# Optimization experiments

Hardware: AMD Instinct MI355X
Metric: run time of the kernel (lower is better)

## Reference

```python
import jax, jax.numpy as jnp
import numpy as np

N = 262144      # number of points
K = 16          # KNN neighbors -> fixed degree CSR
E = N * K
CLASS_DIM = 40


def setup_inputs() -> dict:
    key = jax.random.key(0)
    ks = jax.random.split(key, 12)
    x = jax.random.normal(ks[0], (N, 3), dtype=jnp.float32)
    indptr = (jnp.arange(N + 1, dtype=jnp.int32) * K)
    indices = jax.random.randint(ks[1], (E,), 0, N, dtype=jnp.int32)

    def xavier(k, fan_out, fan_in):
        bound = np.sqrt(6.0 / (fan_in + fan_out)).astype(np.float32)
        return jax.random.uniform(k, (fan_out, fan_in), dtype=jnp.float32,
                                  minval=-bound, maxval=bound)

    return {
        "x": x, "indptr": indptr, "indices": indices,
        "w1": xavier(ks[2], 64, 3),
        "w2": xavier(ks[3], 64, 64),
        "w3": xavier(ks[4], 64, 64),
        "w4": xavier(ks[5], 128, 64),
        "w5": xavier(ks[6], 1024, 192),
        "wf1": xavier(ks[7], 512, 1024),
        "wf2": xavier(ks[8], 256, 512),
        "wf3": xavier(ks[9], CLASS_DIM, 256),
    }


def reference(x, indptr, indices, w1, w2, w3, w4, w5, wf1, wf2, wf3):
    # mlp1, mlp2 (bias-free Linear + ReLU)
    h = jax.nn.relu(x @ w1.T)          # [N, 64]
    h = jax.nn.relu(h @ w2.T)          # [N, 64]

    # GraphMaxPooling: CSR neighbor max (segment-max over gathered rows)
    n = h.shape[0]
    e = indices.shape[0]
    deg = indptr[1:] - indptr[:-1]                                   # [N]
    seg = jnp.repeat(jnp.arange(n, dtype=jnp.int32), deg,
                     total_repeat_length=e)                          # [E]
    x_gm = jax.ops.segment_max(h[indices], seg, num_segments=n,
                               indices_are_sorted=True)              # [N, 64]

    # mlp3, mlp4
    h3 = jax.nn.relu(h @ w3.T)         # [N, 64]
    h4 = jax.nn.relu(h3 @ w4.T)        # [N, 128]

    # concat neighbor-pooled features with point features, mlp5
    hc = jnp.concatenate([x_gm, h4], axis=1)   # [N, 192]
    h5 = jax.nn.relu(hc @ w5.T)                # [N, 1024]

    # global max pool over points -> [1, 1024]
    g = jnp.max(h5, axis=0, keepdims=True)

    # classifier head (dropout in eval mode = identity)
    f = jax.nn.relu(g @ wf1.T)
    f = jax.nn.relu(f @ wf2.T)
    return f @ wf3.T                            # [1, class_dim]
```

## Files before the change

### kernel.cpp

```cpp
#include <hip/hip_runtime.h>
#include <hip/hip_bf16.h>
#include <stdint.h>

typedef unsigned short u16;
typedef __bf16 bf16x8 __attribute__((ext_vector_type(8)));
typedef float  f32x4  __attribute__((ext_vector_type(4)));
typedef u16    u16x8  __attribute__((ext_vector_type(8)));

__device__ __forceinline__ float bf2f(u16 u) {
    return __uint_as_float(((unsigned)u) << 16);
}
__device__ __forceinline__ u16 f2bf(float f) {
    unsigned u = __float_as_uint(f);
    u += 0x7fffu + ((u >> 16) & 1u);
    return (u16)(u >> 16);
}
__device__ __forceinline__ u16x8 maxu16(u16x8 a, u16x8 b) {
    u16x8 r;
    #pragma unroll
    for (int e = 0; e < 8; ++e) r[e] = a[e] > b[e] ? a[e] : b[e];
    return r;
}

#define MFMA16(a, b, c) __builtin_amdgcn_mfma_f32_16x16x32_bf16(a, b, c, 0, 0, 0)

__device__ u16   h2g_buf[262144 * 64];
__device__ u16   gm_buf [262144 * 64];
__device__ u16   w3b[64 * 64];
__device__ u16   w4b[128 * 64];
__device__ u16   w5t[64 * 6 * 64 * 8];
__device__ float g_buf[1024];
__device__ float f1_buf[512];
__device__ float f2_buf[256];

__global__ void k0_zero() { g_buf[threadIdx.x] = 0.f; }

__global__ void kcvt(const float* __restrict__ w3f, const float* __restrict__ w4f,
                     const float* __restrict__ w5f)
{
    int i = blockIdx.x * 256 + threadIdx.x;
    if (i < 4096)        w3b[i]        = f2bf(w3f[i]);
    else if (i < 12288)  w4b[i - 4096] = f2bf(w4f[i - 4096]);
    else {
        int o    = i - 12288;
        int e    = o & 7;
        int lane = (o >> 3) & 63;
        int sg   = o >> 9;
        int s    = sg % 6, c16 = sg / 6;
        int q    = lane >> 4, l15 = lane & 15;
        w5t[o] = f2bf(w5f[(c16 * 16 + l15) * 192 + s * 32 + q * 8 + e]);
    }
}

__global__ __launch_bounds__(256) void k1_mlp(
    const float* __restrict__ xf, const float* __restrict__ w1f,
    const float* __restrict__ w2f)
{
    __shared__ __align__(16) u16 sw1[64 * 4];
    __shared__ __align__(16) u16 sx [64 * 4];
    __shared__ __align__(16) u16 sw2[64 * 72];
    __shared__ __align__(16) u16 shA[64 * 72];
    __shared__ __align__(16) u16 sh2[64 * 72];

    const int tid = threadIdx.x;
    const int p0  = blockIdx.x * 64;

    for (int i = tid; i < 64 * 64; i += 256)
        sw2[(i >> 6) * 72 + (i & 63)] = f2bf(w2f[i]);
    if (tid < 192) {
        sw1[(tid / 3) * 4 + tid % 3] = f2bf(w1f[tid]);
        sx [(tid / 3) * 4 + tid % 3] = f2bf(xf[p0 * 3 + tid]);
    }
    __syncthreads();

    {
        int m = tid & 63, ng = tid >> 6;
        float x0 = bf2f(sx[m * 4]), x1 = bf2f(sx[m * 4 + 1]), x2 = bf2f(sx[m * 4 + 2]);
        #pragma unroll
        for (int j = 0; j < 16; ++j) {
            int n = ng * 16 + j;
            float s = x0 * bf2f(sw1[n * 4]) + x1 * bf2f(sw1[n * 4 + 1]) + x2 * bf2f(sw1[n * 4 + 2]);
            shA[m * 72 + n] = f2bf(fmaxf(s, 0.f));
        }
    }
    __syncthreads();

    const int lane = tid & 63, w = tid >> 6, q = lane >> 4, l15 = lane & 15;
    const int mrow = 16 * w;

    f32x4 acc2[4];
    #pragma unroll
    for (int nt = 0; nt < 4; ++nt) acc2[nt] = (f32x4){0.f, 0.f, 0.f, 0.f};
    #pragma unroll
    for (int s = 0; s < 2; ++s) {
        bf16x8 a = *(const bf16x8*)&shA[(mrow + l15) * 72 + s * 32 + q * 8];
        #pragma unroll
        for (int nt = 0; nt < 4; ++nt) {
            bf16x8 b = *(const bf16x8*)&sw2[(nt * 16 + l15) * 72 + s * 32 + q * 8];
            acc2[nt] = MFMA16(a, b, acc2[nt]);
        }
    }
    #pragma unroll
    for (int nt = 0; nt < 4; ++nt)
        #pragma unroll
        for (int r = 0; r < 4; ++r) {
            int m = mrow + q * 4 + r;
            sh2[m * 72 + nt * 16 + l15] = f2bf(fmaxf(acc2[nt][r], 0.f));
        }
    __syncthreads();

    {
        int row = tid >> 2, c = (tid & 3) * 16;
        *(u16x8*)&h2g_buf[(size_t)p0 * 64 + tid * 16]     = *(const u16x8*)&sh2[row * 72 + c];
        *(u16x8*)&h2g_buf[(size_t)p0 * 64 + tid * 16 + 8] = *(const u16x8*)&sh2[row * 72 + c + 8];
    }
}

__global__ __launch_bounds__(256) void k2_pool(const int* __restrict__ idx)
{
    const size_t gt = (size_t)blockIdx.x * 256 + threadIdx.x;
    const size_t p  = gt >> 3;
    const int    c  = (threadIdx.x & 7) * 8;

    u16x8 v[16];
    #pragma unroll
    for (int k = 0; k < 16; ++k) {
        int j = idx[p * 16 + k];
        v[k] = *(const u16x8*)&h2g_buf[(size_t)j * 64 + c];
    }
    u16x8 m = v[0];
    #pragma unroll
    for (int k = 1; k < 16; ++k) m = maxu16(m, v[k]);
    *(u16x8*)&gm_buf[p * 64 + c] = m;
}

__global__ __launch_bounds__(512) void k3_fused(int* __restrict__ gout)
{
    __shared__ __align__(16) u16 lds[36864];
    u16* p0  = lds;
    u16* p1  = lds + 8192;
    u16* p2  = lds + 16384;
    u16* sw3 = lds + 24576;
    u16* sw4 = lds + 28672;

    const int tid  = threadIdx.x;
    const int lane = tid & 63, w = tid >> 6, q = lane >> 4, l15 = lane & 15;
    const size_t R0 = (size_t)blockIdx.x * 128;

    {
        int r = tid >> 3, js = tid & 7;
        *(u16x8*)&sw3[r * 64 + ((js ^ r) & 7) * 8] = *(const u16x8*)&w3b[r * 64 + js * 8];
        #pragma unroll
        for (int c = 0; c < 2; ++c) {
            int i = c * 512 + tid, r4 = i >> 3, j4 = i & 7;
            *(u16x8*)&sw4[r4 * 64 + ((j4 ^ r4) & 7) * 8] = *(const u16x8*)&w4b[r4 * 64 + j4 * 8];
        }
        #pragma unroll
        for (int c = 0; c < 2; ++c) {
            int i = c * 512 + tid, ra = i >> 3, ja = i & 7;
            *(u16x8*)&p0[ra * 64 + ((ja ^ ra) & 7) * 8] =
                *(const u16x8*)&gm_buf[(R0 + ra) * 64 + ja * 8];
            *(u16x8*)&p1[ra * 64 + ((ja ^ ra) & 7) * 8] =
                *(const u16x8*)&h2g_buf[(R0 + ra) * 64 + ja * 8];
        }
    }
    __syncthreads();

    {
        f32x4 a3[4];
        #pragma unroll
        for (int nt = 0; nt < 4; ++nt) a3[nt] = (f32x4){0.f, 0.f, 0.f, 0.f};
        #pragma unroll
        for (int ss = 0; ss < 2; ++ss) {
            int js = ss * 4 + q, r = w * 16 + l15;
            bf16x8 a = *(const bf16x8*)&p1[r * 64 + ((js ^ r) & 7) * 8];
            #pragma unroll
            for (int nt = 0; nt < 4; ++nt) {
                int rw = nt * 16 + l15;
                bf16x8 b = *(const bf16x8*)&sw3[rw * 64 + ((js ^ rw) & 7) * 8];
                a3[nt] = MFMA16(a, b, a3[nt]);
            }
        }
        #pragma unroll
        for (int nt = 0; nt < 4; ++nt)
            #pragma unroll
            for (int r = 0; r < 4; ++r) {
                int m = w * 16 + q * 4 + r;
                int n = nt * 16 + l15;
                p2[m * 64 + (((n >> 3) ^ m) & 7) * 8 + (n & 7)] =
                    f2bf(fmaxf(a3[nt][r], 0.f));
            }
    }

    {
        f32x4 a4[8];
        #pragma unroll
        for (int nt = 0; nt < 8; ++nt) a4[nt] = (f32x4){0.f, 0.f, 0.f, 0.f};
        #pragma unroll
        for (int ss = 0; ss < 2; ++ss) {
            int js = ss * 4 + q, r = w * 16 + l15;
            bf16x8 a = *(const bf16x8*)&p2[r * 64 + ((js ^ r) & 7) * 8];
            #pragma unroll
            for (int nt = 0; nt < 8; ++nt) {
                int rw = nt * 16 + l15;
                bf16x8 b = *(const bf16x8*)&sw4[rw * 64 + ((js ^ rw) & 7) * 8];
                a4[nt] = MFMA16(a, b, a4[nt]);
            }
        }
        #pragma unroll
        for (int nt = 0; nt < 8; ++nt)
            #pragma unroll
            for (int r = 0; r < 4; ++r) {
                int m  = w * 16 + q * 4 + r;
                int n4 = nt * 16 + l15;
                int j  = (n4 >> 3) & 7;
                u16* dp = (nt < 4) ? p1 : p2;
                dp[m * 64 + ((j ^ m) & 7) * 8 + (n4 & 7)] = f2bf(fmaxf(a4[nt][r], 0.f));
            }
    }
    __syncthreads();

    int zoff = 0;
    #pragma unroll 1
    for (int cg = 0; cg < 4; ++cg) {
        asm volatile("" : "+v"(zoff));
        f32x4 acc[8][2];
        #pragma unroll
        for (int mt = 0; mt < 8; ++mt)
            #pragma unroll
            for (int nt = 0; nt < 2; ++nt) acc[mt][nt] = (f32x4){0.f, 0.f, 0.f, 0.f};
        #pragma unroll
        for (int s = 0; s < 6; ++s) {
            const u16* pa = (s < 2) ? p0 : ((s < 4) ? p1 : p2);
            int j = (s & 1) * 4 + q;
            bf16x8 b[2];
            #pragma unroll
            for (int nt = 0; nt < 2; ++nt)
                b[nt] = *(const bf16x8*)&w5t[(size_t)(((cg * 16 + w * 2 + nt) * 6 + s)) * 512 + lane * 8];
            bf16x8 a[8];
            #pragma unroll
            for (int mt = 0; mt < 8; ++mt) {
                int r = mt * 16 + l15;
                a[mt] = *(const bf16x8*)&pa[r * 64 + ((j ^ r) & 7) * 8 + zoff];
            }
            #pragma unroll
            for (int mt = 0; mt < 8; ++mt)
                #pragma unroll
                for (int nt = 0; nt < 2; ++nt)
                    acc[mt][nt] = MFMA16(a[mt], b[nt], acc[mt][nt]);
        }

        #pragma unroll
        for (int nt = 0; nt < 2; ++nt) {
            float mx = 0.f;
            #pragma unroll
            for (int mt = 0; mt < 8; ++mt)
                #pragma unroll
                for (int e = 0; e < 4; ++e) mx = fmaxf(mx, acc[mt][nt][e]);
            mx = fmaxf(mx, __shfl_xor(mx, 16, 64));
            mx = fmaxf(mx, __shfl_xor(mx, 32, 64));
            if (q == 0)
                atomicMax(&gout[cg * 256 + w * 32 + nt * 16 + l15], __float_as_int(mx));
        }
    }
}

__global__ void k4_f1(const float* __restrict__ wf1)
{
    int r = blockIdx.x, l = threadIdx.x;
    float s = 0.f;
    #pragma unroll
    for (int i = 0; i < 16; ++i) s += wf1[r * 1024 + i * 64 + l] * g_buf[i * 64 + l];
    #pragma unroll
    for (int o = 32; o; o >>= 1) s += __shfl_down(s, o, 64);
    if (!l) f1_buf[r] = fmaxf(s, 0.f);
}
__global__ void k4_f2(const float* __restrict__ wf2)
{
    int r = blockIdx.x, l = threadIdx.x;
    float s = 0.f;
    #pragma unroll
    for (int i = 0; i < 8; ++i) s += wf2[r * 512 + i * 64 + l] * f1_buf[i * 64 + l];
    #pragma unroll
    for (int o = 32; o; o >>= 1) s += __shfl_down(s, o, 64);
    if (!l) f2_buf[r] = fmaxf(s, 0.f);
}
__global__ void k4_out(const float* __restrict__ wf3, float* __restrict__ out)
{
    int r = blockIdx.x, l = threadIdx.x;
    float s = 0.f;
    #pragma unroll
    for (int i = 0; i < 4; ++i) s += wf3[r * 256 + i * 64 + l] * f2_buf[i * 64 + l];
    #pragma unroll
    for (int o = 32; o; o >>= 1) s += __shfl_down(s, o, 64);
    if (!l) out[r] = s;
}

extern "C" void kernel_launch(void* const* d_in, const int* in_sizes, int n_in,
                              void* d_out, int out_size, void* d_ws, size_t ws_size,
                              hipStream_t stream)
{
    (void)in_sizes; (void)n_in; (void)out_size; (void)d_ws; (void)ws_size;
    const float* x   = (const float*)d_in[0];
    const int*   idx = (const int*)d_in[2];
    const float* w1  = (const float*)d_in[3];
    const float* w2  = (const float*)d_in[4];
    const float* w3  = (const float*)d_in[5];
    const float* w4  = (const float*)d_in[6];
    const float* w5  = (const float*)d_in[7];
    const float* wf1 = (const float*)d_in[8];
    const float* wf2 = (const float*)d_in[9];
    const float* wf3 = (const float*)d_in[10];

    float* gptr;
    hipGetSymbolAddress((void**)&gptr, HIP_SYMBOL(g_buf));

    k0_zero <<<1, 1024, 0, stream>>>();
    kcvt    <<<816, 256, 0, stream>>>(w3, w4, w5);
    k1_mlp  <<<262144 / 64, 256, 0, stream>>>(x, w1, w2);
    k2_pool <<<262144 * 8 / 256, 256, 0, stream>>>(idx);
    k3_fused<<<2048, 512, 0, stream>>>((int*)gptr);
    k4_f1   <<<512, 64, 0, stream>>>(wf1);
    k4_f2   <<<256, 64, 0, stream>>>(wf2);
    k4_out  <<<40, 64, 0, stream>>>(wf3, (float*)d_out);
}
```

Before: 388.0 us.

## Switch mlp5 to 32x32x16 MFMA and pre-convert w1/w2 weights once

```diff
diff --git a/kernel.cpp b/kernel.cpp
--- a/kernel.cpp
+++ b/kernel.cpp
@@ -5,6 +5,7 @@
 typedef unsigned short u16;
 typedef __bf16 bf16x8 __attribute__((ext_vector_type(8)));
 typedef float  f32x4  __attribute__((ext_vector_type(4)));
+typedef float  f32x16 __attribute__((ext_vector_type(16)));
 typedef u16    u16x8  __attribute__((ext_vector_type(8)));
 
 __device__ __forceinline__ float bf2f(u16 u) {
@@ -23,38 +24,43 @@
 }
 
 #define MFMA16(a, b, c) __builtin_amdgcn_mfma_f32_16x16x32_bf16(a, b, c, 0, 0, 0)
+#define MFMA32(a, b, c) __builtin_amdgcn_mfma_f32_32x32x16_bf16(a, b, c, 0, 0, 0)
 
 __device__ u16   h2g_buf[262144 * 64];
 __device__ u16   gm_buf [262144 * 64];
+__device__ u16   w1b[64 * 3];
+__device__ u16   w2b[64 * 64];
 __device__ u16   w3b[64 * 64];
 __device__ u16   w4b[128 * 64];
-__device__ u16   w5t[64 * 6 * 64 * 8];
+__device__ u16   w5t[32 * 12 * 64 * 8];
 __device__ float g_buf[1024];
 __device__ float f1_buf[512];
 __device__ float f2_buf[256];
 
 __global__ void k0_zero() { g_buf[threadIdx.x] = 0.f; }
 
-__global__ void kcvt(const float* __restrict__ w3f, const float* __restrict__ w4f,
+__global__ void kcvt(const float* __restrict__ w1f, const float* __restrict__ w2f,
+                     const float* __restrict__ w3f, const float* __restrict__ w4f,
                      const float* __restrict__ w5f)
 {
     int i = blockIdx.x * 256 + threadIdx.x;
-    if (i < 4096)        w3b[i]        = f2bf(w3f[i]);
-    else if (i < 12288)  w4b[i - 4096] = f2bf(w4f[i - 4096]);
-    else {
-        int o    = i - 12288;
+    if (i < 4096)        w3b[i]         = f2bf(w3f[i]);
+    else if (i < 12288)  w4b[i - 4096]  = f2bf(w4f[i - 4096]);
+    else if (i < 12480)  w1b[i - 12288] = f2bf(w1f[i - 12288]);
+    else if (i < 16576)  w2b[i - 12480] = f2bf(w2f[i - 12480]);
+    else if (i < 213184) {
+        int o    = i - 16576;
         int e    = o & 7;
         int lane = (o >> 3) & 63;
-        int sg   = o >> 9;
-        int s    = sg % 6, c16 = sg / 6;
-        int q    = lane >> 4, l15 = lane & 15;
-        w5t[o] = f2bf(w5f[(c16 * 16 + l15) * 192 + s * 32 + q * 8 + e]);
-    }
-}
-
-__global__ __launch_bounds__(256) void k1_mlp(
-    const float* __restrict__ xf, const float* __restrict__ w1f,
-    const float* __restrict__ w2f)
+        int gks  = o >> 9;
+        int ks   = gks % 12, g = gks / 12;
+        int col  = g * 32 + (lane & 31);
+        int k    = ks * 16 + (lane >> 5) * 8 + e;
+        w5t[o] = f2bf(w5f[col * 192 + k]);
+    }
+}
+
+__global__ __launch_bounds__(256) void k1_mlp(const float* __restrict__ xf)
 {
     __shared__ __align__(16) u16 sw1[64 * 4];
     __shared__ __align__(16) u16 sx [64 * 4];
@@ -65,10 +71,14 @@
     const int tid = threadIdx.x;
     const int p0  = blockIdx.x * 64;
 
-    for (int i = tid; i < 64 * 64; i += 256)
-        sw2[(i >> 6) * 72 + (i & 63)] = f2bf(w2f[i]);
+    #pragma unroll
+    for (int c = 0; c < 2; ++c) {
+        int ch = c * 256 + tid;
+        int row = ch >> 3, j = ch & 7;
+        *(u16x8*)&sw2[row * 72 + j * 8] = *(const u16x8*)&w2b[row * 64 + j * 8];
+    }
     if (tid < 192) {
-        sw1[(tid / 3) * 4 + tid % 3] = f2bf(w1f[tid]);
+        sw1[(tid / 3) * 4 + tid % 3] = w1b[tid];
         sx [(tid / 3) * 4 + tid % 3] = f2bf(xf[p0 * 3 + tid]);
     }
     __syncthreads();
@@ -220,48 +230,40 @@
     }
     __syncthreads();
 
+    const int l31 = lane & 31, hi = lane >> 5;
     int zoff = 0;
     #pragma unroll 1
     for (int cg = 0; cg < 4; ++cg) {
         asm volatile("" : "+v"(zoff));
-        f32x4 acc[8][2];
-        #pragma unroll
-        for (int mt = 0; mt < 8; ++mt)
-            #pragma unroll
-            for (int nt = 0; nt < 2; ++nt) acc[mt][nt] = (f32x4){0.f, 0.f, 0.f, 0.f};
-        #pragma unroll
-        for (int s = 0; s < 6; ++s) {
-            const u16* pa = (s < 2) ? p0 : ((s < 4) ? p1 : p2);
-            int j = (s & 1) * 4 + q;
-            bf16x8 b[2];
-            #pragma unroll
-            for (int nt = 0; nt < 2; ++nt)
-                b[nt] = *(const bf16x8*)&w5t[(size_t)(((cg * 16 + w * 2 + nt) * 6 + s)) * 512 + lane * 8];
-            bf16x8 a[8];
-            #pragma unroll
-            for (int mt = 0; mt < 8; ++mt) {
-                int r = mt * 16 + l15;
+        f32x16 acc[4];
+        #pragma unroll
+        for (int mt = 0; mt < 4; ++mt) acc[mt] = (f32x16)(0.f);
+        #pragma unroll
+        for (int ks = 0; ks < 12; ++ks) {
+            const u16* pa = (ks < 4) ? p0 : ((ks < 8) ? p1 : p2);
+            int j = (ks & 3) * 2 + hi;
+            bf16x8 b = *(const bf16x8*)&w5t[(size_t)((cg * 8 + w) * 12 + ks) * 512 + lane * 8];
+            bf16x8 a[4];
+            #pragma unroll
+            for (int mt = 0; mt < 4; ++mt) {
+                int r = mt * 32 + l31;
                 a[mt] = *(const bf16x8*)&pa[r * 64 + ((j ^ r) & 7) * 8 + zoff];
             }
-            #pragma unroll
-            for (int mt = 0; mt < 8; ++mt)
-                #pragma unroll
-                for (int nt = 0; nt < 2; ++nt)
-                    acc[mt][nt] = MFMA16(a[mt], b[nt], acc[mt][nt]);
-        }
-
-        #pragma unroll
-        for (int nt = 0; nt < 2; ++nt) {
-            float mx = 0.f;
-            #pragma unroll
-            for (int mt = 0; mt < 8; ++mt)
-                #pragma unroll
-                for (int e = 0; e < 4; ++e) mx = fmaxf(mx, acc[mt][nt][e]);
-            mx = fmaxf(mx, __shfl_xor(mx, 16, 64));
-            mx = fmaxf(mx, __shfl_xor(mx, 32, 64));
-            if (q == 0)
-                atomicMax(&gout[cg * 256 + w * 32 + nt * 16 + l15], __float_as_int(mx));
-        }
+            __builtin_amdgcn_s_setprio(1);
+            #pragma unroll
+            for (int mt = 0; mt < 4; ++mt)
+                acc[mt] = MFMA32(a[mt], b, acc[mt]);
+            __builtin_amdgcn_s_setprio(0);
+        }
+
+        float mx = 0.f;
+        #pragma unroll
+        for (int mt = 0; mt < 4; ++mt)
+            #pragma unroll
+            for (int e = 0; e < 16; ++e) mx = fmaxf(mx, acc[mt][e]);
+        mx = fmaxf(mx, __shfl_xor(mx, 32, 64));
+        if (hi == 0)
+            atomicMax(&gout[cg * 256 + w * 32 + l31], __float_as_int(mx));
     }
 }
 
@@ -316,8 +318,8 @@
     hipGetSymbolAddress((void**)&gptr, HIP_SYMBOL(g_buf));
 
     k0_zero <<<1, 1024, 0, stream>>>();
-    kcvt    <<<816, 256, 0, stream>>>(w3, w4, w5);
-    k1_mlp  <<<262144 / 64, 256, 0, stream>>>(x, w1, w2);
+    kcvt    <<<833, 256, 0, stream>>>(w1, w2, w3, w4, w5);
+    k1_mlp  <<<262144 / 64, 256, 0, stream>>>(x);
     k2_pool <<<262144 * 8 / 256, 256, 0, stream>>>(idx);
     k3_fused<<<2048, 512, 0, stream>>>((int*)gptr);
     k4_f1   <<<512, 64, 0, stream>>>(wf1);
```

New measurement: 384.4 us. Within noise of the previous version (-0.9%).
